# Kernel tuning notes

Measured on AMD Instinct MI355X. Metric: run time of the kernel, lower is better.

Reference implementation:

```python
import jax, jax.numpy as jnp
import numpy as np

N_NODES = 100000
EPS = 1e-5  # BatchNorm1d default


def gcn_conv(x, W, b, edge_index, n_nodes):
    """PyG GCNConv: add self-loops, symmetric deg^-1/2 normalization,
    aggregate source messages at destination, then add bias."""
    src, dst = edge_index[0], edge_index[1]
    loop = jnp.arange(n_nodes, dtype=src.dtype)
    src = jnp.concatenate([src, loop])
    dst = jnp.concatenate([dst, loop])
    deg = jax.ops.segment_sum(jnp.ones_like(dst, dtype=x.dtype), dst,
                              num_segments=n_nodes)
    dinv = jnp.where(deg > 0, jax.lax.rsqrt(deg), 0.0)
    norm = dinv[src] * dinv[dst]  # [E+N]
    h = x @ W  # [N, out]
    msg = h[src] * norm[:, None]  # [E+N, out]
    out = jax.ops.segment_sum(msg, dst, num_segments=n_nodes)
    return out + b


def batch_norm(x, gamma, beta):
    # training-mode BatchNorm1d: biased batch statistics over the node dim
    mean = jnp.mean(x, axis=0)
    var = jnp.mean(jnp.square(x - mean), axis=0)
    return (x - mean) * jax.lax.rsqrt(var + EPS) * gamma + beta


def setup_inputs() -> dict:
    key = jax.random.key(0)
    ks = jax.random.split(key, 6)
    in_c, out_c = 128, 64
    hid = 2 * out_c
    n_edges = 1600000
    x = jax.random.normal(ks[0], (N_NODES, in_c), dtype=jnp.float32)
    edge_index = jax.random.randint(ks[1], (2, n_edges), 0, N_NODES,
                                    dtype=jnp.int32)
    # glorot-style init for GCN weights, zero bias
    W1 = jax.random.normal(ks[2], (in_c, hid), dtype=jnp.float32) / np.sqrt(in_c)
    b1 = jnp.zeros((hid,), dtype=jnp.float32)
    W2 = jax.random.normal(ks[3], (hid, out_c), dtype=jnp.float32) / np.sqrt(hid)
    b2 = jnp.zeros((out_c,), dtype=jnp.float32)
    gamma1 = jnp.ones((hid,), dtype=jnp.float32)
    beta1 = jnp.zeros((hid,), dtype=jnp.float32)
    gamma2 = jnp.ones((out_c,), dtype=jnp.float32)
    beta2 = jnp.zeros((out_c,), dtype=jnp.float32)
    return {"x": x, "W1": W1, "b1": b1, "gamma1": gamma1, "beta1": beta1,
            "W2": W2, "b2": b2, "gamma2": gamma2, "beta2": beta2,
            "edge_index": edge_index}


def reference(x, W1, b1, gamma1, beta1, W2, b2, gamma2, beta2, edge_index):
    n = x.shape[0]
    h = gcn_conv(x, W1, b1, edge_index, n)
    h = jax.nn.relu(batch_norm(h, gamma1, beta1))
    h = gcn_conv(h, W2, b2, edge_index, n)
    return batch_norm(h, gamma2, beta2)
```

## Files before the change

kernel.cpp:

```cpp
#include <hip/hip_runtime.h>

#define WS_ALIGN(x) (((x) + size_t(255)) & ~size_t(255))

typedef unsigned int uint;
typedef unsigned short ushort;
typedef __attribute__((ext_vector_type(8))) short short8;
typedef __attribute__((ext_vector_type(4))) float floatx4;

#define SHIFT 9
#define NPB   (1 << SHIFT)
#define CRB   1024

__device__ __forceinline__ ushort f2bf(float f) {
    uint u = __float_as_uint(f);
    return (ushort)((u + 0x7fff + ((u >> 16) & 1)) >> 16);
}
__device__ __forceinline__ float bflo(uint u) { return __uint_as_float(u << 16); }
__device__ __forceinline__ float bfhi(uint u) { return __uint_as_float(u & 0xffff0000u); }
__device__ __forceinline__ float bf1(ushort s) { return __uint_as_float(((uint)s) << 16); }


__global__ __launch_bounds__(256) void p1_hist(const int* __restrict__ dst, int E,
                                               int chunk, int NB, int* __restrict__ ghist) {
    __shared__ int h[256];
    h[threadIdx.x] = 0;
    __syncthreads();
    int e0 = blockIdx.x * chunk, e1 = min(E, e0 + chunk);
    for (int e = e0 + threadIdx.x; e < e1; e += 256)
        atomicAdd(&h[dst[e] >> SHIFT], 1);
    __syncthreads();
    if ((int)threadIdx.x < NB) ghist[blockIdx.x * NB + threadIdx.x] = h[threadIdx.x];
}

__global__ __launch_bounds__(256) void p1_colscan(int* __restrict__ ghist, int NB,
                                                  int* __restrict__ tot) {
    __shared__ int lds[256];
    int c = blockIdx.x, t = threadIdx.x;
    int v = (t < NB) ? ghist[t * NB + c] : 0;
    lds[t] = v;
    __syncthreads();
    for (int o = 1; o < 256; o <<= 1) {
        int u = (t >= o) ? lds[t - o] : 0;
        __syncthreads();
        if (t >= o) lds[t] += u;
        __syncthreads();
    }
    if (t < NB) ghist[t * NB + c] = lds[t] - v;
    if (t == 255) tot[c] = lds[255];
}

__global__ __launch_bounds__(256) void p1_base(const int* __restrict__ tot, int NB,
                                               int* __restrict__ bbase) {
    __shared__ int lds[256];
    int t = threadIdx.x;
    int v = (t < NB) ? tot[t] : 0;
    lds[t] = v;
    __syncthreads();
    for (int o = 1; o < 256; o <<= 1) {
        int u = (t >= o) ? lds[t - o] : 0;
        __syncthreads();
        if (t >= o) lds[t] += u;
        __syncthreads();
    }
    if (t < NB) bbase[t] = lds[t] - v;
    if (t == 255) bbase[NB] = lds[255];
}

__global__ __launch_bounds__(256) void p1_place(const int* __restrict__ src,
                                                const int* __restrict__ dst, int E,
                                                int chunk, int NB,
                                                const int* __restrict__ ghist,
                                                const int* __restrict__ bbase,
                                                int* __restrict__ parts) {
    __shared__ int h[256];
    __shared__ int base[256];
    int t = threadIdx.x;
    h[t] = 0;
    if (t < NB) base[t] = bbase[t] + ghist[blockIdx.x * NB + t];
    __syncthreads();
    int e0 = blockIdx.x * chunk, e1 = min(E, e0 + chunk);
    for (int e = e0 + t; e < e1; e += 256) {
        int d = dst[e];
        int b = d >> SHIFT;
        int local = atomicAdd(&h[b], 1);
        parts[base[b] + local] = src[e] | ((d & (NPB - 1)) << 17);
    }
}

__global__ __launch_bounds__(256) void p2_csr(const int* __restrict__ parts,
                                              const int* __restrict__ bbase, int N,
                                              int* __restrict__ nodeStart,
                                              int* __restrict__ nodeCnt,
                                              int* __restrict__ esrc) {
    __shared__ int cnt[NPB], off[NPB], cur[NPB];
    __shared__ int pair[256];
    int b = blockIdx.x, t = threadIdx.x;
    int n0 = b << SHIFT;
    cnt[t] = 0;
    cnt[t + 256] = 0;
    cur[t] = 0;
    cur[t + 256] = 0;
    __syncthreads();
    int e0 = bbase[b], e1 = bbase[b + 1];
    for (int e = e0 + t; e < e1; e += 256)
        atomicAdd(&cnt[(parts[e] >> 17) & (NPB - 1)], 1);
    __syncthreads();
    int psum = cnt[2 * t] + cnt[2 * t + 1];
    pair[t] = psum;
    __syncthreads();
    for (int o = 1; o < 256; o <<= 1) {
        int u = (t >= o) ? pair[t - o] : 0;
        __syncthreads();
        if (t >= o) pair[t] += u;
        __syncthreads();
    }
    int excl = pair[t] - psum;
    off[2 * t] = excl;
    off[2 * t + 1] = excl + cnt[2 * t];
    __syncthreads();
#pragma unroll
    for (int j = t; j < NPB; j += 256) {
        int n = n0 + j;
        if (n < N) {
            nodeStart[n] = e0 + off[j];
            nodeCnt[n] = cnt[j];
        }
    }
    for (int e = e0 + t; e < e1; e += 256) {
        int p = parts[e];
        int dl = (p >> 17) & (NPB - 1);
        int local = atomicAdd(&cur[dl], 1);
        esrc[e0 + off[dl] + local] = p & 0x1FFFF;
    }
}

__global__ void dinv_kernel(const int* __restrict__ cnt, float* __restrict__ dinv, int N) {
    int i = blockIdx.x * blockDim.x + threadIdx.x;
    if (i < N) dinv[i] = rsqrtf((float)(cnt[i] + 1));
}


__global__ void wconv(const float* __restrict__ W1, const float* __restrict__ W2,
                      ushort* __restrict__ W1t, ushort* __restrict__ W2t) {
    int i = blockIdx.x * blockDim.x + threadIdx.x;
    if (i < 128 * 128) {
        int n = i >> 7, k = i & 127;
        W1t[i] = f2bf(W1[k * 128 + n]);
    }
    int j = i - 128 * 128;
    if (j >= 0 && j < 64 * 128) {
        int n = j >> 7, k = j & 127;
        W2t[j] = f2bf(W2[k * 64 + n]);
    }
}


template <int TN, bool BN>
__global__ __launch_bounds__(256) void gemm_mfma(const float* __restrict__ A,
                                                 const ushort* __restrict__ Wt,
                                                 const float* __restrict__ scale,
                                                 const float* __restrict__ shift,
                                                 const float* __restrict__ dinv,
                                                 ushort* __restrict__ Cb, int M) {
    constexpr int TM = 64;
    constexpr int PK = 136;
    constexpr int NCT = TN / 16;
    __shared__ ushort Ab[TM * PK];
    __shared__ ushort Wl[TN * PK];
    int tid = threadIdx.x;
    int wave = tid >> 6, lane = tid & 63;
    int rowBase = blockIdx.x * TM;

    for (int l = tid; l < TN * 16; l += 256) {
        int n = l >> 4, c = (l & 15) << 3;
        *(uint4*)&Wl[n * PK + c] = *(const uint4*)&Wt[n * 128 + c];
    }
    for (int l = tid; l < TM * 32; l += 256) {
        int r = l >> 5, c = (l & 31) << 2;
        int gr = rowBase + r;
        float4 v = make_float4(0.f, 0.f, 0.f, 0.f);
        if (gr < M) v = *(const float4*)&A[(size_t)gr * 128 + c];
        if (BN) {
            v.x = fmaxf(fmaf(v.x, scale[c + 0], shift[c + 0]), 0.f);
            v.y = fmaxf(fmaf(v.y, scale[c + 1], shift[c + 1]), 0.f);
            v.z = fmaxf(fmaf(v.z, scale[c + 2], shift[c + 2]), 0.f);
            v.w = fmaxf(fmaf(v.w, scale[c + 3], shift[c + 3]), 0.f);
        }
        uint2 p;
        p.x = (uint)f2bf(v.x) | ((uint)f2bf(v.y) << 16);
        p.y = (uint)f2bf(v.z) | ((uint)f2bf(v.w) << 16);
        *(uint2*)&Ab[r * PK + c] = p;
    }
    __syncthreads();

    floatx4 acc[NCT];
#pragma unroll
    for (int ct = 0; ct < NCT; ++ct) acc[ct] = (floatx4){0.f, 0.f, 0.f, 0.f};

    int m = wave * 16 + (lane & 15);
    int quad = lane >> 4;
#pragma unroll
    for (int kc = 0; kc < 128; kc += 32) {
        int k0 = kc + quad * 8;
        short8 a = *(const short8*)&Ab[m * PK + k0];
#pragma unroll
        for (int ct = 0; ct < NCT; ++ct) {
            short8 b = *(const short8*)&Wl[(ct * 16 + (lane & 15)) * PK + k0];
            acc[ct] = __builtin_amdgcn_mfma_f32_16x16x32_bf16(a, b, acc[ct], 0, 0, 0);
        }
    }

    int r0 = rowBase + wave * 16 + quad * 4;
    int col0 = lane & 15;
#pragma unroll
    for (int r = 0; r < 4; ++r) {
        int gr = r0 + r;
        if (gr < M) {
            float dv = dinv[gr];
#pragma unroll
            for (int ct = 0; ct < NCT; ++ct)
                Cb[(size_t)gr * TN + ct * 16 + col0] = f2bf(acc[ct][r] * dv);
        }
    }
}


__global__ __launch_bounds__(256) void spmm128(const ushort* __restrict__ hb,
                                               const int* __restrict__ nodeStart,
                                               const int* __restrict__ nodeCnt,
                                               const int* __restrict__ esrc,
                                               const float* __restrict__ dinv,
                                               float* __restrict__ out, int N) {
    int node = blockIdx.x * 4 + (threadIdx.x >> 6);
    if (node >= N) return;
    int lane = threadIdx.x & 63;
    int par = lane >> 5;
    int c = lane & 31;
    const uint2* hp2 = (const uint2*)hb;
    uint2 sv = hp2[(size_t)node * 32 + c];
    float a0, a1, a2, a3;
    if (par == 0) { a0 = bflo(sv.x); a1 = bfhi(sv.x); a2 = bflo(sv.y); a3 = bfhi(sv.y); }
    else          { a0 = 0.f; a1 = 0.f; a2 = 0.f; a3 = 0.f; }
    float b0 = 0.f, b1 = 0.f, b2 = 0.f, b3 = 0.f;
    int cnt = nodeCnt[node];
    const int* bp = esrc + nodeStart[node];
    int e = 0;
    if (cnt >= 16) {
        int s[8];
#pragma unroll
        for (int j = 0; j < 8; ++j) s[j] = bp[2 * j + par];
        while (true) {
            int sn[8];
#pragma unroll
            for (int j = 0; j < 8; ++j) sn[j] = bp[e + 16 + 2 * j + par];
            uint2 u[8];
#pragma unroll
            for (int j = 0; j < 8; ++j) u[j] = hp2[(size_t)s[j] * 32 + c];
#pragma unroll
            for (int j = 0; j < 8; ++j) {
                if (j & 1) { b0 += bflo(u[j].x); b1 += bfhi(u[j].x);
                             b2 += bflo(u[j].y); b3 += bfhi(u[j].y); }
                else       { a0 += bflo(u[j].x); a1 += bfhi(u[j].x);
                             a2 += bflo(u[j].y); a3 += bfhi(u[j].y); }
            }
            e += 16;
            if (e + 16 > cnt) break;
#pragma unroll
            for (int j = 0; j < 8; ++j) s[j] = sn[j];
        }
    }
    if (e < cnt) {
        int last = cnt - 1;
        int s[8];
#pragma unroll
        for (int j = 0; j < 8; ++j) {
            int o = e + 2 * j + par;
            s[j] = bp[o < cnt ? o : last];
        }
        uint2 u[8];
#pragma unroll
        for (int j = 0; j < 8; ++j) u[j] = hp2[(size_t)s[j] * 32 + c];
#pragma unroll
        for (int j = 0; j < 8; ++j) {
            bool ok = (e + 2 * j + par) < cnt;
            if (j & 1) { b0 += ok ? bflo(u[j].x) : 0.f; b1 += ok ? bfhi(u[j].x) : 0.f;
                         b2 += ok ? bflo(u[j].y) : 0.f; b3 += ok ? bfhi(u[j].y) : 0.f; }
            else       { a0 += ok ? bflo(u[j].x) : 0.f; a1 += ok ? bfhi(u[j].x) : 0.f;
                         a2 += ok ? bflo(u[j].y) : 0.f; a3 += ok ? bfhi(u[j].y) : 0.f; }
        }
    }
    a0 += b0; a1 += b1; a2 += b2; a3 += b3;
    a0 += __shfl_xor(a0, 32);
    a1 += __shfl_xor(a1, 32);
    a2 += __shfl_xor(a2, 32);
    a3 += __shfl_xor(a3, 32);
    if (par == 0) {
        float dv = dinv[node];
        ((float4*)out)[(size_t)node * 32 + c] =
            make_float4(dv * a0, dv * a1, dv * a2, dv * a3);
    }
}

__global__ __launch_bounds__(256) void spmm64(const ushort* __restrict__ hb,
                                              const int* __restrict__ nodeStart,
                                              const int* __restrict__ nodeCnt,
                                              const int* __restrict__ esrc,
                                              const float* __restrict__ dinv,
                                              float* __restrict__ out, int N) {
    int node = blockIdx.x * 4 + (threadIdx.x >> 6);
    if (node >= N) return;
    int lane = threadIdx.x & 63;
    int par = lane >> 5;
    int c = lane & 31;
    const uint* hp = (const uint*)hb;
    uint sv = hp[(size_t)node * 32 + c];
    float a0, a1;
    if (par == 0) { a0 = bflo(sv); a1 = bfhi(sv); }
    else          { a0 = 0.f; a1 = 0.f; }
    float b0 = 0.f, b1 = 0.f;
    int cnt = nodeCnt[node];
    const int* bp = esrc + nodeStart[node];
    int e = 0;
    if (cnt >= 16) {
        int s[8];
#pragma unroll
        for (int j = 0; j < 8; ++j) s[j] = bp[2 * j + par];
        while (true) {
            int sn[8];
#pragma unroll
            for (int j = 0; j < 8; ++j) sn[j] = bp[e + 16 + 2 * j + par];
            uint u[8];
#pragma unroll
            for (int j = 0; j < 8; ++j) u[j] = hp[(size_t)s[j] * 32 + c];
#pragma unroll
            for (int j = 0; j < 8; ++j) {
                if (j & 1) { b0 += bflo(u[j]); b1 += bfhi(u[j]); }
                else       { a0 += bflo(u[j]); a1 += bfhi(u[j]); }
            }
            e += 16;
            if (e + 16 > cnt) break;
#pragma unroll
            for (int j = 0; j < 8; ++j) s[j] = sn[j];
        }
    }
    if (e < cnt) {
        int last = cnt - 1;
        int s[8];
#pragma unroll
        for (int j = 0; j < 8; ++j) {
            int o = e + 2 * j + par;
            s[j] = bp[o < cnt ? o : last];
        }
        uint u[8];
#pragma unroll
        for (int j = 0; j < 8; ++j) u[j] = hp[(size_t)s[j] * 32 + c];
#pragma unroll
        for (int j = 0; j < 8; ++j) {
            bool ok = (e + 2 * j + par) < cnt;
            if (j & 1) { b0 += ok ? bflo(u[j]) : 0.f; b1 += ok ? bfhi(u[j]) : 0.f; }
            else       { a0 += ok ? bflo(u[j]) : 0.f; a1 += ok ? bfhi(u[j]) : 0.f; }
        }
    }
    a0 += b0; a1 += b1;
    a0 += __shfl_xor(a0, 32);
    a1 += __shfl_xor(a1, 32);
    if (par == 0) {
        float dv = dinv[node];
        ((float2*)out)[(size_t)node * 32 + c] = make_float2(dv * a0, dv * a1);
    }
}


template <int F>
__global__ __launch_bounds__(256) void col_partial(const float* __restrict__ a, int M,
                                                   float* __restrict__ partials) {
    constexpr int C4 = F / 4;
    constexpr int RPI = 256 / C4;
    int col4 = threadIdx.x % C4;
    int rsub = threadIdx.x / C4;
    const float4* a4 = (const float4*)a;
    float sx = 0.f, sy = 0.f, sz = 0.f, sw = 0.f;
    float qx = 0.f, qy = 0.f, qz = 0.f, qw = 0.f;
    for (int r = blockIdx.x * RPI + rsub; r < M; r += gridDim.x * RPI) {
        float4 v = a4[(size_t)r * C4 + col4];
        sx += v.x; sy += v.y; sz += v.z; sw += v.w;
        qx += v.x * v.x; qy += v.y * v.y; qz += v.z * v.z; qw += v.w * v.w;
    }
    __shared__ float4 ls[256], lq[256];
    ls[threadIdx.x] = make_float4(sx, sy, sz, sw);
    lq[threadIdx.x] = make_float4(qx, qy, qz, qw);
    __syncthreads();
    if (rsub == 0) {
        for (int t = col4 + C4; t < 256; t += C4) {
            float4 s2 = ls[t], q2 = lq[t];
            sx += s2.x; sy += s2.y; sz += s2.z; sw += s2.w;
            qx += q2.x; qy += q2.y; qz += q2.z; qw += q2.w;
        }
        float4* ps = (float4*)(partials + (size_t)blockIdx.x * 2 * F);
        ps[col4] = make_float4(sx, sy, sz, sw);
        ps[C4 + col4] = make_float4(qx, qy, qz, qw);
    }
}

template <int F>
__global__ __launch_bounds__(1024) void col_finish(const float* __restrict__ partials,
                                                   int M,
                                                   const float* __restrict__ gamma,
                                                   const float* __restrict__ beta,
                                                   float* __restrict__ scale,
                                                   float* __restrict__ shift) {
    constexpr int C = 2 * F;
    constexpr int C4 = C / 4;
    constexpr int NCH = 1024 / C4;
    int t = threadIdx.x;
    int col4 = t % C4;
    int chunk = t / C4;
    const float4* p4 = (const float4*)partials;
    float4 a0 = make_float4(0.f, 0.f, 0.f, 0.f), a1 = a0, a2 = a0, a3 = a0;
    for (int b = chunk; b < CRB; b += 4 * NCH) {
        float4 v0 = p4[(size_t)(b + 0 * NCH) * C4 + col4];
        float4 v1 = p4[(size_t)(b + 1 * NCH) * C4 + col4];
        float4 v2 = p4[(size_t)(b + 2 * NCH) * C4 + col4];
        float4 v3 = p4[(size_t)(b + 3 * NCH) * C4 + col4];
        a0.x += v0.x; a0.y += v0.y; a0.z += v0.z; a0.w += v0.w;
        a1.x += v1.x; a1.y += v1.y; a1.z += v1.z; a1.w += v1.w;
        a2.x += v2.x; a2.y += v2.y; a2.z += v2.z; a2.w += v2.w;
        a3.x += v3.x; a3.y += v3.y; a3.z += v3.z; a3.w += v3.w;
    }
    a0.x += a1.x + a2.x + a3.x;
    a0.y += a1.y + a2.y + a3.y;
    a0.z += a1.z + a2.z + a3.z;
    a0.w += a1.w + a2.w + a3.w;
    __shared__ float4 red[1024];
    red[t] = a0;
    __syncthreads();
    __shared__ float fin[C];
    if (t < C4) {
        float4 s = red[t];
        for (int k = 1; k < NCH; ++k) {
            float4 v = red[t + k * C4];
            s.x += v.x; s.y += v.y; s.z += v.z; s.w += v.w;
        }
        fin[t * 4 + 0] = s.x;
        fin[t * 4 + 1] = s.y;
        fin[t * 4 + 2] = s.z;
        fin[t * 4 + 3] = s.w;
    }
    __syncthreads();
    if (t < F) {
        float mean = fin[t] / (float)M;
        float var = fin[F + t] / (float)M - mean * mean;
        float iv = rsqrtf(var + 1e-5f);
        float sc = gamma[t] * iv;
        scale[t] = sc;
        shift[t] = beta[t] - mean * sc;
    }
}

__global__ void apply_bn64(const float* __restrict__ a, const float* __restrict__ scale,
                           const float* __restrict__ shift, float* __restrict__ out, int n4) {
    int i = blockIdx.x * blockDim.x + threadIdx.x;
    if (i >= n4) return;
    float4 v = ((const float4*)a)[i];
    int c0 = (i & 15) * 4;
    float4 sc = *(const float4*)&scale[c0];
    float4 sh = *(const float4*)&shift[c0];
    v.x = fmaf(v.x, sc.x, sh.x);
    v.y = fmaf(v.y, sc.y, sh.y);
    v.z = fmaf(v.z, sc.z, sh.z);
    v.w = fmaf(v.w, sc.w, sh.w);
    ((float4*)out)[i] = v;
}


extern "C" void kernel_launch(void* const* d_in, const int* in_sizes, int n_in,
                              void* d_out, int out_size, void* d_ws, size_t ws_size,
                              hipStream_t stream) {
    const float* x      = (const float*)d_in[0];
    const float* W1     = (const float*)d_in[1];
    const float* gamma1 = (const float*)d_in[3];
    const float* beta1  = (const float*)d_in[4];
    const float* W2     = (const float*)d_in[5];
    const float* gamma2 = (const float*)d_in[7];
    const float* beta2  = (const float*)d_in[8];
    const int*   ei     = (const int*)d_in[9];

    const int hid  = in_sizes[2];
    const int outc = in_sizes[6];
    const int inc  = in_sizes[1] / hid;
    const int N    = in_sizes[0] / inc;
    const int E    = in_sizes[9] / 2;
    const int* srcp = ei;
    const int* dstp = ei + E;
    const int NB   = (N + NPB - 1) >> SHIFT;
    const int chunk = (E + NB - 1) / NB;

    char* wsp = (char*)d_ws;
    size_t off = 0;
    auto alloc = [&](size_t bytes) -> void* {
        void* p = wsp + off;
        off += WS_ALIGN(bytes);
        return p;
    };
    int*   ghist    = (int*)alloc((size_t)NB * NB * 4);
    int*   tot      = (int*)alloc((size_t)NB * 4);
    int*   bbase    = (int*)alloc((size_t)(NB + 1) * 4);
    int*   parts    = (int*)alloc((size_t)E * 4);
    int*   esrc     = (int*)alloc((size_t)(E + 16) * 4);
    int*   nodeStart= (int*)alloc((size_t)N * 4);
    int*   nodeCnt  = (int*)alloc((size_t)N * 4);
    float* dinv     = (float*)alloc((size_t)N * 4);
    float* part1    = (float*)alloc((size_t)CRB * 2 * hid * 4);
    float* part2    = (float*)alloc((size_t)CRB * 2 * outc * 4);
    float* scale1   = (float*)alloc((size_t)hid * 4);
    float* shift1   = (float*)alloc((size_t)hid * 4);
    float* scale2   = (float*)alloc((size_t)outc * 4);
    float* shift2   = (float*)alloc((size_t)outc * 4);
    ushort* W1t     = (ushort*)alloc((size_t)hid * inc * 2);
    ushort* W2t     = (ushort*)alloc((size_t)outc * hid * 2);
    ushort* h1b     = (ushort*)alloc((size_t)N * hid * 2);
    float* agg1     = (float*)alloc((size_t)N * hid * 4);
    ushort* h2b     = h1b;
    float* agg2     = agg1;

    p1_hist<<<NB, 256, 0, stream>>>(dstp, E, chunk, NB, ghist);
    p1_colscan<<<NB, 256, 0, stream>>>(ghist, NB, tot);
    p1_base<<<1, 256, 0, stream>>>(tot, NB, bbase);
    p1_place<<<NB, 256, 0, stream>>>(srcp, dstp, E, chunk, NB, ghist, bbase, parts);
    p2_csr<<<NB, 256, 0, stream>>>(parts, bbase, N, nodeStart, nodeCnt, esrc);
    dinv_kernel<<<(N + 255) / 256, 256, 0, stream>>>(nodeCnt, dinv, N);
    wconv<<<(128 * 128 + 64 * 128 + 255) / 256, 256, 0, stream>>>(W1, W2, W1t, W2t);

    gemm_mfma<128, false><<<(N + 63) / 64, 256, 0, stream>>>(x, W1t, nullptr, nullptr,
                                                             dinv, h1b, N);
    spmm128<<<(N + 3) / 4, 256, 0, stream>>>(h1b, nodeStart, nodeCnt, esrc, dinv, agg1, N);
    col_partial<128><<<CRB, 256, 0, stream>>>(agg1, N, part1);
    col_finish<128><<<1, 1024, 0, stream>>>(part1, N, gamma1, beta1, scale1, shift1);

    gemm_mfma<64, true><<<(N + 63) / 64, 256, 0, stream>>>(agg1, W2t, scale1, shift1,
                                                           dinv, h2b, N);
    spmm64<<<(N + 3) / 4, 256, 0, stream>>>(h2b, nodeStart, nodeCnt, esrc, dinv, agg2, N);
    col_partial<64><<<CRB, 256, 0, stream>>>(agg2, N, part2);
    col_finish<64><<<1, 1024, 0, stream>>>(part2, N, gamma2, beta2, scale2, shift2);
    apply_bn64<<<(N * 64 / 4 + 255) / 256, 256, 0, stream>>>(agg2, scale2, shift2,
                                                             (float*)d_out, N * 64 / 4);
}
```

Measured before the change: 358.4 us.

## Fuse batch-norm column statistics into SpMM and widen gathers to 16-byte loads

```diff
diff --git a/kernel.cpp b/kernel.cpp
--- a/kernel.cpp
+++ b/kernel.cpp
@@ -17,7 +17,6 @@
 }
 __device__ __forceinline__ float bflo(uint u) { return __uint_as_float(u << 16); }
 __device__ __forceinline__ float bfhi(uint u) { return __uint_as_float(u & 0xffff0000u); }
-__device__ __forceinline__ float bf1(ushort s) { return __uint_as_float(((uint)s) << 16); }
 
 
 __global__ __launch_bounds__(256) void p1_hist(const int* __restrict__ dst, int E,
@@ -230,74 +229,112 @@
                                                const int* __restrict__ nodeCnt,
                                                const int* __restrict__ esrc,
                                                const float* __restrict__ dinv,
-                                               float* __restrict__ out, int N) {
-    int node = blockIdx.x * 4 + (threadIdx.x >> 6);
-    if (node >= N) return;
-    int lane = threadIdx.x & 63;
-    int par = lane >> 5;
-    int c = lane & 31;
-    const uint2* hp2 = (const uint2*)hb;
-    uint2 sv = hp2[(size_t)node * 32 + c];
-    float a0, a1, a2, a3;
-    if (par == 0) { a0 = bflo(sv.x); a1 = bfhi(sv.x); a2 = bflo(sv.y); a3 = bfhi(sv.y); }
-    else          { a0 = 0.f; a1 = 0.f; a2 = 0.f; a3 = 0.f; }
-    float b0 = 0.f, b1 = 0.f, b2 = 0.f, b3 = 0.f;
-    int cnt = nodeCnt[node];
-    const int* bp = esrc + nodeStart[node];
-    int e = 0;
-    if (cnt >= 16) {
-        int s[8];
-#pragma unroll
-        for (int j = 0; j < 8; ++j) s[j] = bp[2 * j + par];
-        while (true) {
-            int sn[8];
-#pragma unroll
-            for (int j = 0; j < 8; ++j) sn[j] = bp[e + 16 + 2 * j + par];
-            uint2 u[8];
-#pragma unroll
-            for (int j = 0; j < 8; ++j) u[j] = hp2[(size_t)s[j] * 32 + c];
-#pragma unroll
-            for (int j = 0; j < 8; ++j) {
-                if (j & 1) { b0 += bflo(u[j].x); b1 += bfhi(u[j].x);
-                             b2 += bflo(u[j].y); b3 += bfhi(u[j].y); }
-                else       { a0 += bflo(u[j].x); a1 += bfhi(u[j].x);
-                             a2 += bflo(u[j].y); a3 += bfhi(u[j].y); }
-            }
-            e += 16;
-            if (e + 16 > cnt) break;
-#pragma unroll
-            for (int j = 0; j < 8; ++j) s[j] = sn[j];
-        }
-    }
-    if (e < cnt) {
-        int last = cnt - 1;
-        int s[8];
-#pragma unroll
-        for (int j = 0; j < 8; ++j) {
-            int o = e + 2 * j + par;
-            s[j] = bp[o < cnt ? o : last];
-        }
-        uint2 u[8];
-#pragma unroll
-        for (int j = 0; j < 8; ++j) u[j] = hp2[(size_t)s[j] * 32 + c];
-#pragma unroll
-        for (int j = 0; j < 8; ++j) {
-            bool ok = (e + 2 * j + par) < cnt;
-            if (j & 1) { b0 += ok ? bflo(u[j].x) : 0.f; b1 += ok ? bfhi(u[j].x) : 0.f;
-                         b2 += ok ? bflo(u[j].y) : 0.f; b3 += ok ? bfhi(u[j].y) : 0.f; }
-            else       { a0 += ok ? bflo(u[j].x) : 0.f; a1 += ok ? bfhi(u[j].x) : 0.f;
-                         a2 += ok ? bflo(u[j].y) : 0.f; a3 += ok ? bfhi(u[j].y) : 0.f; }
-        }
-    }
-    a0 += b0; a1 += b1; a2 += b2; a3 += b3;
-    a0 += __shfl_xor(a0, 32);
-    a1 += __shfl_xor(a1, 32);
-    a2 += __shfl_xor(a2, 32);
-    a3 += __shfl_xor(a3, 32);
+                                               float* __restrict__ out, int N,
+                                               float* __restrict__ partials) {
+    int wid = threadIdx.x >> 6, lane = threadIdx.x & 63;
+    int par = lane >> 4;
+    int cc = lane & 15;
+    const char* hbase = (const char*)hb;
+    float sacc[8], qacc[8];
+#pragma unroll
+    for (int i = 0; i < 8; ++i) { sacc[i] = 0.f; qacc[i] = 0.f; }
+    int stride = gridDim.x * 4;
+    for (int node = blockIdx.x * 4 + wid; node < N; node += stride) {
+        float a[8];
+        {
+            uint4 sv = make_uint4(0, 0, 0, 0);
+            if (par == 0)
+                sv = *(const uint4*)(hbase + (((uint)node << 8) + (cc << 4)));
+            a[0] = bflo(sv.x); a[1] = bfhi(sv.x);
+            a[2] = bflo(sv.y); a[3] = bfhi(sv.y);
+            a[4] = bflo(sv.z); a[5] = bfhi(sv.z);
+            a[6] = bflo(sv.w); a[7] = bfhi(sv.w);
+        }
+        int cnt = nodeCnt[node];
+        const int* bp = esrc + nodeStart[node];
+        int e = 0;
+        if (cnt >= 16) {
+            int s[4];
+#pragma unroll
+            for (int j = 0; j < 4; ++j) s[j] = bp[4 * j + par];
+            while (true) {
+                int sn[4];
+#pragma unroll
+                for (int j = 0; j < 4; ++j) sn[j] = bp[e + 16 + 4 * j + par];
+                uint4 u[4];
+#pragma unroll
+                for (int j = 0; j < 4; ++j)
+                    u[j] = *(const uint4*)(hbase + (((uint)s[j] << 8) + (cc << 4)));
+#pragma unroll
+                for (int j = 0; j < 4; ++j) {
+                    a[0] += bflo(u[j].x); a[1] += bfhi(u[j].x);
+                    a[2] += bflo(u[j].y); a[3] += bfhi(u[j].y);
+                    a[4] += bflo(u[j].z); a[5] += bfhi(u[j].z);
+                    a[6] += bflo(u[j].w); a[7] += bfhi(u[j].w);
+                }
+                e += 16;
+                if (e + 16 > cnt) break;
+#pragma unroll
+                for (int j = 0; j < 4; ++j) s[j] = sn[j];
+            }
+        }
+        if (e < cnt) {
+            int last = cnt - 1;
+            int s[4];
+#pragma unroll
+            for (int j = 0; j < 4; ++j) {
+                int o = e + 4 * j + par;
+                s[j] = bp[o < cnt ? o : last];
+            }
+            uint4 u[4];
+#pragma unroll
+            for (int j = 0; j < 4; ++j)
+                u[j] = *(const uint4*)(hbase + (((uint)s[j] << 8) + (cc << 4)));
+#pragma unroll
+            for (int j = 0; j < 4; ++j) {
+                float m = ((e + 4 * j + par) < cnt) ? 1.f : 0.f;
+                a[0] += m * bflo(u[j].x); a[1] += m * bfhi(u[j].x);
+                a[2] += m * bflo(u[j].y); a[3] += m * bfhi(u[j].y);
+                a[4] += m * bflo(u[j].z); a[5] += m * bfhi(u[j].z);
+                a[6] += m * bflo(u[j].w); a[7] += m * bfhi(u[j].w);
+            }
+        }
+#pragma unroll
+        for (int i = 0; i < 8; ++i) {
+            a[i] += __shfl_xor(a[i], 16);
+            a[i] += __shfl_xor(a[i], 32);
+        }
+        if (par == 0) {
+            float dv = dinv[node];
+            float r[8];
+#pragma unroll
+            for (int i = 0; i < 8; ++i) {
+                r[i] = dv * a[i];
+                sacc[i] += r[i];
+                qacc[i] += r[i] * r[i];
+            }
+            float4* op = ((float4*)out) + (((size_t)node) << 5) + (cc << 1);
+            op[0] = make_float4(r[0], r[1], r[2], r[3]);
+            op[1] = make_float4(r[4], r[5], r[6], r[7]);
+        }
+    }
+    __shared__ float sred[4][128], qred[4][128];
     if (par == 0) {
-        float dv = dinv[node];
-        ((float4*)out)[(size_t)node * 32 + c] =
-            make_float4(dv * a0, dv * a1, dv * a2, dv * a3);
+#pragma unroll
+        for (int i = 0; i < 8; ++i) {
+            sred[wid][cc * 8 + i] = sacc[i];
+            qred[wid][cc * 8 + i] = qacc[i];
+        }
+    }
+    __syncthreads();
+    int t = threadIdx.x;
+    if (t < 128) {
+        partials[(size_t)blockIdx.x * 256 + t] =
+            sred[0][t] + sred[1][t] + sred[2][t] + sred[3][t];
+    } else {
+        int c = t - 128;
+        partials[(size_t)blockIdx.x * 256 + t] =
+            qred[0][c] + qred[1][c] + qred[2][c] + qred[3][c];
     }
 }
 
@@ -306,99 +343,113 @@
                                               const int* __restrict__ nodeCnt,
                                               const int* __restrict__ esrc,
                                               const float* __restrict__ dinv,
-                                              float* __restrict__ out, int N) {
-    int node = blockIdx.x * 4 + (threadIdx.x >> 6);
-    if (node >= N) return;
-    int lane = threadIdx.x & 63;
-    int par = lane >> 5;
-    int c = lane & 31;
-    const uint* hp = (const uint*)hb;
-    uint sv = hp[(size_t)node * 32 + c];
-    float a0, a1;
-    if (par == 0) { a0 = bflo(sv); a1 = bfhi(sv); }
-    else          { a0 = 0.f; a1 = 0.f; }
-    float b0 = 0.f, b1 = 0.f;
-    int cnt = nodeCnt[node];
-    const int* bp = esrc + nodeStart[node];
-    int e = 0;
-    if (cnt >= 16) {
-        int s[8];
-#pragma unroll
-        for (int j = 0; j < 8; ++j) s[j] = bp[2 * j + par];
-        while (true) {
-            int sn[8];
-#pragma unroll
-            for (int j = 0; j < 8; ++j) sn[j] = bp[e + 16 + 2 * j + par];
-            uint u[8];
-#pragma unroll
-            for (int j = 0; j < 8; ++j) u[j] = hp[(size_t)s[j] * 32 + c];
-#pragma unroll
-            for (int j = 0; j < 8; ++j) {
-                if (j & 1) { b0 += bflo(u[j]); b1 += bfhi(u[j]); }
-                else       { a0 += bflo(u[j]); a1 += bfhi(u[j]); }
-            }
-            e += 16;
-            if (e + 16 > cnt) break;
-#pragma unroll
-            for (int j = 0; j < 8; ++j) s[j] = sn[j];
-        }
-    }
-    if (e < cnt) {
-        int last = cnt - 1;
-        int s[8];
-#pragma unroll
-        for (int j = 0; j < 8; ++j) {
-            int o = e + 2 * j + par;
-            s[j] = bp[o < cnt ? o : last];
-        }
-        uint u[8];
-#pragma unroll
-        for (int j = 0; j < 8; ++j) u[j] = hp[(size_t)s[j] * 32 + c];
-#pragma unroll
-        for (int j = 0; j < 8; ++j) {
-            bool ok = (e + 2 * j + par) < cnt;
-            if (j & 1) { b0 += ok ? bflo(u[j]) : 0.f; b1 += ok ? bfhi(u[j]) : 0.f; }
-            else       { a0 += ok ? bflo(u[j]) : 0.f; a1 += ok ? bfhi(u[j]) : 0.f; }
-        }
-    }
-    a0 += b0; a1 += b1;
-    a0 += __shfl_xor(a0, 32);
-    a1 += __shfl_xor(a1, 32);
+                                              float* __restrict__ out, int N,
+                                              float* __restrict__ partials) {
+    int wid = threadIdx.x >> 6, lane = threadIdx.x & 63;
+    int par = lane >> 3;
+    int cc = lane & 7;
+    const char* hbase = (const char*)hb;
+    float sacc[8], qacc[8];
+#pragma unroll
+    for (int i = 0; i < 8; ++i) { sacc[i] = 0.f; qacc[i] = 0.f; }
+    int stride = gridDim.x * 4;
+    for (int node = blockIdx.x * 4 + wid; node < N; node += stride) {
+        float a[8];
+        {
+            uint4 sv = make_uint4(0, 0, 0, 0);
+            if (par == 0)
+                sv = *(const uint4*)(hbase + (((uint)node << 7) + (cc << 4)));
+            a[0] = bflo(sv.x); a[1] = bfhi(sv.x);
+            a[2] = bflo(sv.y); a[3] = bfhi(sv.y);
+            a[4] = bflo(sv.z); a[5] = bfhi(sv.z);
+            a[6] = bflo(sv.w); a[7] = bfhi(sv.w);
+        }
+        int cnt = nodeCnt[node];
+        const int* bp = esrc + nodeStart[node];
+        int e = 0;
+        if (cnt >= 16) {
+            int s[2];
+#pragma unroll
+            for (int j = 0; j < 2; ++j) s[j] = bp[8 * j + par];
+            while (true) {
+                int sn[2];
+#pragma unroll
+                for (int j = 0; j < 2; ++j) sn[j] = bp[e + 16 + 8 * j + par];
+                uint4 u[2];
+#pragma unroll
+                for (int j = 0; j < 2; ++j)
+                    u[j] = *(const uint4*)(hbase + (((uint)s[j] << 7) + (cc << 4)));
+#pragma unroll
+                for (int j = 0; j < 2; ++j) {
+                    a[0] += bflo(u[j].x); a[1] += bfhi(u[j].x);
+                    a[2] += bflo(u[j].y); a[3] += bfhi(u[j].y);
+                    a[4] += bflo(u[j].z); a[5] += bfhi(u[j].z);
+                    a[6] += bflo(u[j].w); a[7] += bfhi(u[j].w);
+                }
+                e += 16;
+                if (e + 16 > cnt) break;
+#pragma unroll
+                for (int j = 0; j < 2; ++j) s[j] = sn[j];
+            }
+        }
+        if (e < cnt) {
+            int last = cnt - 1;
+            int s[2];
+#pragma unroll
+            for (int j = 0; j < 2; ++j) {
+                int o = e + 8 * j + par;
+                s[j] = bp[o < cnt ? o : last];
+            }
+            uint4 u[2];
+#pragma unroll
+            for (int j = 0; j < 2; ++j)
+                u[j] = *(const uint4*)(hbase + (((uint)s[j] << 7) + (cc << 4)));
+#pragma unroll
+            for (int j = 0; j < 2; ++j) {
+                float m = ((e + 8 * j + par) < cnt) ? 1.f : 0.f;
+                a[0] += m * bflo(u[j].x); a[1] += m * bfhi(u[j].x);
+                a[2] += m * bflo(u[j].y); a[3] += m * bfhi(u[j].y);
+                a[4] += m * bflo(u[j].z); a[5] += m * bfhi(u[j].z);
+                a[6] += m * bflo(u[j].w); a[7] += m * bfhi(u[j].w);
+            }
+        }
+#pragma unroll
+        for (int i = 0; i < 8; ++i) {
+            a[i] += __shfl_xor(a[i], 8);
+            a[i] += __shfl_xor(a[i], 16);
+            a[i] += __shfl_xor(a[i], 32);
+        }
+        if (par == 0) {
+            float dv = dinv[node];
+            float r[8];
+#pragma unroll
+            for (int i = 0; i < 8; ++i) {
+                r[i] = dv * a[i];
+                sacc[i] += r[i];
+                qacc[i] += r[i] * r[i];
+            }
+            float4* op = ((float4*)out) + (((size_t)node) << 4) + (cc << 1);
+            op[0] = make_float4(r[0], r[1], r[2], r[3]);
+            op[1] = make_float4(r[4], r[5], r[6], r[7]);
+        }
+    }
+    __shared__ float sred[4][64], qred[4][64];
     if (par == 0) {
-        float dv = dinv[node];
-        ((float2*)out)[(size_t)node * 32 + c] = make_float2(dv * a0, dv * a1);
-    }
-}
-
-
-template <int F>
-__global__ __launch_bounds__(256) void col_partial(const float* __restrict__ a, int M,
-                                                   float* __restrict__ partials) {
-    constexpr int C4 = F / 4;
-    constexpr int RPI = 256 / C4;
-    int col4 = threadIdx.x % C4;
-    int rsub = threadIdx.x / C4;
-    const float4* a4 = (const float4*)a;
-    float sx = 0.f, sy = 0.f, sz = 0.f, sw = 0.f;
-    float qx = 0.f, qy = 0.f, qz = 0.f, qw = 0.f;
-    for (int r = blockIdx.x * RPI + rsub; r < M; r += gridDim.x * RPI) {
-        float4 v = a4[(size_t)r * C4 + col4];
-        sx += v.x; sy += v.y; sz += v.z; sw += v.w;
-        qx += v.x * v.x; qy += v.y * v.y; qz += v.z * v.z; qw += v.w * v.w;
-    }
-    __shared__ float4 ls[256], lq[256];
-    ls[threadIdx.x] = make_float4(sx, sy, sz, sw);
-    lq[threadIdx.x] = make_float4(qx, qy, qz, qw);
-    __syncthreads();
-    if (rsub == 0) {
-        for (int t = col4 + C4; t < 256; t += C4) {
-            float4 s2 = ls[t], q2 = lq[t];
-            sx += s2.x; sy += s2.y; sz += s2.z; sw += s2.w;
-            qx += q2.x; qy += q2.y; qz += q2.z; qw += q2.w;
-        }
-        float4* ps = (float4*)(partials + (size_t)blockIdx.x * 2 * F);
-        ps[col4] = make_float4(sx, sy, sz, sw);
-        ps[C4 + col4] = make_float4(qx, qy, qz, qw);
+#pragma unroll
+        for (int i = 0; i < 8; ++i) {
+            sred[wid][cc * 8 + i] = sacc[i];
+            qred[wid][cc * 8 + i] = qacc[i];
+        }
+    }
+    __syncthreads();
+    int t = threadIdx.x;
+    if (t < 64) {
+        partials[(size_t)blockIdx.x * 128 + t] =
+            sred[0][t] + sred[1][t] + sred[2][t] + sred[3][t];
+    } else if (t < 128) {
+        int c = t - 64;
+        partials[(size_t)blockIdx.x * 128 + t] =
+            qred[0][c] + qred[1][c] + qred[2][c] + qred[3][c];
     }
 }
 
@@ -533,14 +584,12 @@
 
     gemm_mfma<128, false><<<(N + 63) / 64, 256, 0, stream>>>(x, W1t, nullptr, nullptr,
                                                              dinv, h1b, N);
-    spmm128<<<(N + 3) / 4, 256, 0, stream>>>(h1b, nodeStart, nodeCnt, esrc, dinv, agg1, N);
-    col_partial<128><<<CRB, 256, 0, stream>>>(agg1, N, part1);
+    spmm128<<<CRB, 256, 0, stream>>>(h1b, nodeStart, nodeCnt, esrc, dinv, agg1, N, part1);
     col_finish<128><<<1, 1024, 0, stream>>>(part1, N, gamma1, beta1, scale1, shift1);
 
     gemm_mfma<64, true><<<(N + 63) / 64, 256, 0, stream>>>(agg1, W2t, scale1, shift1,
                                                            dinv, h2b, N);
-    spmm64<<<(N + 3) / 4, 256, 0, stream>>>(h2b, nodeStart, nodeCnt, esrc, dinv, agg2, N);
-    col_partial<64><<<CRB, 256, 0, stream>>>(agg2, N, part2);
+    spmm64<<<CRB, 256, 0, stream>>>(h2b, nodeStart, nodeCnt, esrc, dinv, agg2, N, part2);
     col_finish<64><<<1, 1024, 0, stream>>>(part2, N, gamma2, beta2, scale2, shift2);
     apply_bn64<<<(N * 64 / 4 + 255) / 256, 256, 0, stream>>>(agg2, scale2, shift2,
                                                              (float*)d_out, N * 64 / 4);
```

Result: slower. 370.0 us (+3.3%).
